# Kernel optimization log

Hardware: AMD Instinct MI355X
Metric: run time of the kernel (lower is better)

Reference implementation:

```python
import jax, jax.numpy as jnp
from jax import lax
import numpy as np

WAY = 100
SHOT = 5
QUERY = 15
D = 4096
LAM = 10.0
ALPHA = 0.2
N_EPOCHS = 20
EPS = 1e-6
MAXITERS = 1000
N_L = WAY * SHOT          # 500 labeled
N_U = WAY * QUERY         # 1500 unlabeled
N_TOT = N_L + N_U         # 2000


def setup_inputs() -> dict:
    key = jax.random.key(0)
    kx, = jax.random.split(key, 1)
    X = jax.random.uniform(kx, (N_TOT, D), dtype=jnp.float32)  # features must be >= 0
    # data is ordered as (shot+query) blocks of `way` samples, one per class
    labels = jnp.tile(jnp.arange(WAY, dtype=jnp.int32), SHOT + QUERY)
    return {"X": X, "labels": labels}


def _normalize(X):
    # F.normalize(p=2, dim=-1) with eps=1e-12
    return X / jnp.maximum(jnp.linalg.norm(X, axis=-1, keepdims=True), 1e-12)


def _cdist(X, Y):
    # Euclidean distances [n, m] via gram trick (avoids [n, m, d] intermediate)
    d2 = (X * X).sum(-1)[:, None] + (Y * Y).sum(-1)[None, :] - 2.0 * (X @ Y.T)
    return jnp.sqrt(jnp.maximum(d2, 1e-12))


def _sinkhorn(M, r, c):
    # Row/col scaling loop of compute_optimal_transport, tracked via scaling
    # vectors (a, b) so P_k = a * K * b exactly matches the in-place updates.
    K = jnp.exp(-LAM * M)
    K = K / K.sum()
    n, m = M.shape

    def step(carry, _):
        a, b, prev, done = carry
        rowsum = a * (K @ b)                       # P.sum(-1)
        err = jnp.max(jnp.abs(prev - rowsum))      # convergence check vs old u
        done = done | (err <= EPS)
        a_new = jnp.where(done, a, a * r / rowsum)
        colsum = b * (K.T @ a_new)                 # P.sum(1) after row scaling
        b_new = jnp.where(done, b, b * c / colsum)
        prev_new = jnp.where(done, prev, rowsum)
        return (a_new, b_new, prev_new, done), None

    init = (jnp.ones(n, M.dtype), jnp.ones(m, M.dtype),
            jnp.zeros(n, M.dtype), jnp.array(False))
    (a, b, _, _), _ = lax.scan(step, init, None, length=MAXITERS)
    return a[:, None] * K * b[None, :]


def _forward(X, labels):
    # power transform
    X = jnp.sqrt(X + 1e-6)
    # scale (mode='val'): normalize -> center labeled/unlabeled separately -> normalize
    X = _normalize(X)
    Xl = X[:N_L] - X[:N_L].mean(0, keepdims=True)
    Xu = X[N_L:] - X[N_L:].mean(0, keepdims=True)
    Z = _normalize(jnp.concatenate([Xl, Xu], axis=0))

    # init class means from labeled shots
    mus0 = Z.reshape(SHOT + QUERY, WAY, -1)[:SHOT].mean(0)  # [way, d]

    r = jnp.ones(N_U, Z.dtype)
    c = jnp.full((WAY,), float(QUERY), Z.dtype)
    onehot = jax.nn.one_hot(labels[:N_L], WAY, dtype=Z.dtype)

    def get_probas(mus):
        dist = _cdist(Z, mus)                      # [n_tot, way]
        Pu = _sinkhorn(dist[N_L:], r, c)           # [n_u, way]
        return jnp.concatenate([onehot, Pu], axis=0)

    def epoch(mus, _):
        p = get_probas(mus)
        emus = (p.T @ Z) / p.sum(0)[:, None]       # estimate_from_mask
        return mus + ALPHA * (emus - mus), None    # update_from_estimate

    mus, _ = lax.scan(epoch, mus0, None, length=N_EPOCHS)

    P = get_probas(mus)
    logP = jnp.log(P[N_L:] + 1e-5)
    acc = (jnp.argmax(P[N_L:], axis=-1) == labels[N_L:]).astype(jnp.float32).mean()
    return logP, acc


def reference(X, labels):
    return _forward(X, labels)
```

## Files before the change

### kernel.cpp

```cpp
#include <hip/hip_runtime.h>

#define WAY   100
#define SHOT  5
#define NQ    15
#define DD    4096
#define N_L   500
#define N_U   1500
#define N_TOT 2000
#define LAMF  10.0f
#define EPSF  1e-6f
#define MAXIT 1000

#define OFF_Z      0u
#define OFF_CPP    3145728u
#define OFF_MEANL  8192000u
#define OFF_MEANU  8196096u
#define OFF_SL     8200192u
#define OFF_MUSA   8609792u
#define OFF_MUSB   9068544u
#define OFF_MUSQP  9527296u
#define OFF_MUSB16 9552896u
#define OFF_PTH    9782272u
#define OFF_PTL    9868288u
#define OFF_KMAT   9954304u
#define OFF_COLS   10104320u
#define OFF_MISC   10113920u
#define OFF_ZUT    10114688u
#define OFF_ZUTL   13260416u
#define OFF_AG     16406144u
#define OFF_PREVG  16407680u
#define OFF_BINIT  16409216u

#define SINK_BLOCKS 16
#define SINK_T 512
#define RPB 94
#define CPR 12
#define PTS 1536
#define CPS 409600u

typedef __attribute__((ext_vector_type(8))) short short8_t;
typedef __attribute__((ext_vector_type(4))) float f32x4;

__device__ __forceinline__ short f2bs(float f) {
  unsigned u = __float_as_uint(f);
  unsigned r = (u + 0x7FFFu + ((u >> 16) & 1u)) >> 16;
  return (short)r;
}
__device__ __forceinline__ float bs2f(short s) {
  return __uint_as_float(((unsigned)(unsigned short)s) << 16);
}

__device__ __forceinline__ float ld_agent(const float* p) {
  return __hip_atomic_load(p, __ATOMIC_RELAXED, __HIP_MEMORY_SCOPE_AGENT);
}
__device__ __forceinline__ void st_agent(float* p, float v) {
  __hip_atomic_store(p, v, __ATOMIC_RELAXED, __HIP_MEMORY_SCOPE_AGENT);
}

__global__ __launch_bounds__(256) void k_pow_norm(const float* __restrict__ X, float* __restrict__ Z,
                                                  float* __restrict__ msums, unsigned* __restrict__ misc_u,
                                                  float* __restrict__ aG) {
  int i = blockIdx.x, tid = threadIdx.x;
  __shared__ float red[256];
  if (i < 32) msums[i * 256 + tid] = 0.f;
  if (i == 32) { misc_u[tid] = 0u; misc_u[tid + 256] = 0u; misc_u[tid + 512] = 0u; }
  if (i == 33) { for (int z = tid; z < 1504; z += 256) aG[z] = -1.f; }
  const float* x = X + (size_t)i * DD;
  float s = 0.f;
  for (int k = tid; k < DD; k += 256) s += x[k] + 1e-6f;
  red[tid] = s; __syncthreads();
  for (int o = 128; o > 0; o >>= 1) { if (tid < o) red[tid] += red[tid + o]; __syncthreads(); }
  float inv = 1.0f / fmaxf(sqrtf(red[0]), 1e-12f);
  float* z = Z + (size_t)i * DD;
  for (int k = tid; k < DD; k += 256) z[k] = sqrtf(x[k] + 1e-6f) * inv;
}

__global__ __launch_bounds__(256) void k_colmeans(const float* __restrict__ Z, float* __restrict__ mLs,
                                                  float* __restrict__ mUs) {
  int k = blockIdx.x * 256 + threadIdx.x;
  int r0 = blockIdx.y * 80;
  float sL = 0.f, sU = 0.f;
  for (int r = r0; r < r0 + 80; ++r) {
    float v = Z[(size_t)r * DD + k];
    if (r < N_L) sL += v; else sU += v;
  }
  if (r0 < N_L) atomicAdd(&mLs[k], sL);
  if (r0 + 80 > N_L) atomicAdd(&mUs[k], sU);
}

__global__ __launch_bounds__(256) void k_center(float* __restrict__ Z, const float* __restrict__ mLs,
                                                const float* __restrict__ mUs) {
  int i = blockIdx.x, tid = threadIdx.x;
  __shared__ float red[256];
  const float* m = (i < N_L) ? mLs : mUs;
  const float scale = (i < N_L) ? (1.0f / 500.0f) : (1.0f / 1500.0f);
  float* z = Z + (size_t)i * DD;
  float s = 0.f;
  for (int k = tid; k < DD; k += 256) { float v = z[k] - m[k] * scale; s += v * v; }
  red[tid] = s; __syncthreads();
  for (int o = 128; o > 0; o >>= 1) { if (tid < o) red[tid] += red[tid + o]; __syncthreads(); }
  float inv = 1.0f / fmaxf(sqrtf(red[0]), 1e-12f);
  for (int k = tid; k < DD; k += 256) z[k] = (z[k] - m[k] * scale) * inv;
}

__global__ __launch_bounds__(256) void k_musinit(const float* __restrict__ Z, float* __restrict__ SL,
                                                 float* __restrict__ mus, short* __restrict__ musb,
                                                 float* __restrict__ musqP, float* __restrict__ binit) {
  int w = blockIdx.x, tid = threadIdx.x;
  __shared__ float red[256];
  if (tid == 0) binit[w] = 1.0f;
  float q = 0.f;
  for (int k = tid; k < DD; k += 256) {
    float s = 0.f;
    for (int sh = 0; sh < SHOT; ++sh) s += Z[(size_t)(sh * WAY + w) * DD + k];
    SL[(size_t)w * DD + k] = s;
    float m = s / 5.0f;
    mus[(size_t)w * DD + k] = m;
    musb[(size_t)w * DD + k] = f2bs(m);
    q += m * m;
  }
  red[tid] = q; __syncthreads();
  for (int o = 128; o > 0; o >>= 1) { if (tid < o) red[tid] += red[tid + o]; __syncthreads(); }
  if (tid == 0) musqP[(size_t)w * 256] = red[0];
  else musqP[(size_t)w * 256 + tid] = 0.f;
}

__global__ __launch_bounds__(256) void k_zb(const float* __restrict__ Z, short* __restrict__ Zb, int ubase) {
  size_t i0 = (size_t)ubase * DD + ((size_t)blockIdx.x * 256 + threadIdx.x) * 8;
  short8_t v;
  if (i0 < (size_t)N_U * DD) {
    const float* src = Z + (size_t)N_L * DD + i0;
    float4 a = *(const float4*)src;
    float4 b = *(const float4*)(src + 4);
    v[0] = f2bs(a.x); v[1] = f2bs(a.y); v[2] = f2bs(a.z); v[3] = f2bs(a.w);
    v[4] = f2bs(b.x); v[5] = f2bs(b.y); v[6] = f2bs(b.z); v[7] = f2bs(b.w);
  } else {
    v = (short8_t){0, 0, 0, 0, 0, 0, 0, 0};
  }
  *(short8_t*)(Zb + i0) = v;
}

__global__ __launch_bounds__(256) void k_zt(const float* __restrict__ Z, short* __restrict__ ZTH,
                                            short* __restrict__ ZTL) {
  __shared__ float tile[32][33];
  int k0 = blockIdx.x * 32, u0 = blockIdx.y * 32;
  int c = threadIdx.x & 31, r0 = threadIdx.x >> 5;
#pragma unroll
  for (int rr = 0; rr < 4; ++rr) {
    int r = r0 + rr * 8;
    int u = u0 + r;
    tile[r][c] = (u < N_U) ? Z[(size_t)(N_L + u) * DD + k0 + c] : 0.f;
  }
  __syncthreads();
#pragma unroll
  for (int rr = 0; rr < 4; ++rr) {
    int r = r0 + rr * 8;
    float v = tile[c][r];
    short hi = f2bs(v);
    ZTH[(size_t)(k0 + r) * PTS + u0 + c] = hi;
    ZTL[(size_t)(k0 + r) * PTS + u0 + c] = f2bs(v - bs2f(hi));
  }
}

__global__ __launch_bounds__(256) void k_gemm1K(const short* __restrict__ Zb, const short* __restrict__ musb,
                                                const float* __restrict__ musqP, float* __restrict__ Kmat,
                                                unsigned* __restrict__ misc_u) {
  int tid = threadIdx.x;
  __shared__ float redA[4 * 7 * 4 * 64];
  __shared__ float musq2[2][128];
  if (blockIdx.x == 0) {
    for (int z = tid; z < 768; z += 256) misc_u[z] = 0u;
  }
  {
    int w = tid >> 1, half = tid & 1;
    if (w < WAY) {
      const float* mp = musqP + (size_t)w * 256 + half * 128;
      float q = 0.f;
#pragma unroll 4
      for (int bb = 0; bb < 128; bb += 4) {
        float4 v4 = *(const float4*)(mp + bb);
        q += (v4.x + v4.y) + (v4.z + v4.w);
      }
      musq2[half][w] = q;
    }
  }
  int wv = tid >> 6, l = tid & 63;
  int l15 = l & 15, quad = (l >> 4) & 3;
  int u0 = blockIdx.x * 16;
  f32x4 acc[7];
#pragma unroll
  for (int c = 0; c < 7; ++c) acc[c] = (f32x4){0.f, 0.f, 0.f, 0.f};

  const short* bp = Zb + (size_t)(u0 + l15) * DD + wv * 1024 + quad * 8;
  const short* ap = musb + (size_t)l15 * DD + wv * 1024 + quad * 8;
#pragma unroll 2
  for (int kc = 0; kc < 1024; kc += 32) {
    short8_t bf = *(const short8_t*)(bp + kc);
#pragma unroll
    for (int c = 0; c < 7; ++c) {
      short8_t af = *(const short8_t*)(ap + (size_t)c * 16 * DD + kc);
      acc[c] = __builtin_amdgcn_mfma_f32_16x16x32_bf16(af, bf, acc[c], 0, 0, 0);
    }
  }
#pragma unroll
  for (int c = 0; c < 7; ++c)
#pragma unroll
    for (int r = 0; r < 4; ++r)
      redA[((wv * 7 + c) * 4 + r) * 64 + l] = acc[c][r];
  __syncthreads();
  if (wv == 0) {
    int u = u0 + l15;
#pragma unroll
    for (int c = 0; c < 7; ++c)
#pragma unroll
      for (int r = 0; r < 4; ++r) {
        int base = (c * 4 + r) * 64 + l;
        float s = redA[base] + redA[base + 1792] + redA[base + 3584] + redA[base + 5376];
        int w = 16 * c + quad * 4 + r;
        if (w < WAY && u < N_U) {
          float d2 = 1.0f + (musq2[0][w] + musq2[1][w]) - 2.0f * s;
          Kmat[(size_t)u * WAY + w] = expf(-LAMF * sqrtf(fmaxf(d2, 1e-12f)));
        }
      }
  }
}

__device__ __forceinline__ void gbar(unsigned* slots, unsigned t) {
  __syncthreads();
  if (threadIdx.x == 0) {
    asm volatile("s_waitcnt vmcnt(0) lgkmcnt(0)" ::: "memory");
    __hip_atomic_store(slots + (unsigned)blockIdx.x * 16, t, __ATOMIC_RELAXED, __HIP_MEMORY_SCOPE_AGENT);
  }
  if (threadIdx.x < SINK_BLOCKS) {
    while (__hip_atomic_load(slots + threadIdx.x * 16, __ATOMIC_ACQUIRE, __HIP_MEMORY_SCOPE_AGENT) < t)
      __builtin_amdgcn_s_sleep(1);
  }
  __syncthreads();
}

__global__ __launch_bounds__(SINK_T) void k_sink(const float* __restrict__ Kg,
                                                 short* __restrict__ PTH, short* __restrict__ PTL,
                                                 float* __restrict__ colsP, float* __restrict__ aG,
                                                 float* __restrict__ prevG, float* __restrict__ binit,
                                                 unsigned* __restrict__ misc_u, float* __restrict__ misc_f,
                                                 const int* __restrict__ labels, float* __restrict__ out,
                                                 int finalmode) {
  __shared__ float Kl[RPB * 100];
  __shared__ float4 bS4[25];
  __shared__ float a[RPB], aold[RPB], prevs[RPB];
  __shared__ float rerr[SINK_T];
  __shared__ float c2[800];
  __shared__ float red[SINK_T];
  __shared__ float eSh;
  float* bS = (float*)bS4;
  unsigned* slots = misc_u + 8;
  float* KsumG = misc_f + 3;
  int tid = threadIdx.x;
  int row0 = (int)blockIdx.x * RPB;
  int nrows = (blockIdx.x == SINK_BLOCKS - 1) ? (N_U - row0) : RPB;

  float ks = 0.f;
  int n4 = nrows * 25;
  const float4* Ksrc = (const float4*)(Kg + (size_t)row0 * 100);
  for (int i = tid; i < n4; i += SINK_T) {
    float4 v = Ksrc[i];
    *(float4*)(&Kl[i * 4]) = v;
    ks += (v.x + v.y) + (v.z + v.w);
  }
  red[tid] = ks; __syncthreads();
  for (int o = SINK_T / 2; o > 0; o >>= 1) { if (tid < o) red[tid] += red[tid + o]; __syncthreads(); }
  if (tid == 0) atomicAdd(KsumG, red[0]);
  if (tid < WAY) bS[tid] = binit[tid];

  bool warm = (aG[row0] >= 0.f);
  unsigned bt = 0;
  if (!warm) { ++bt; gbar(slots, bt); }
  float S = warm ? 1.f : ld_agent(KsumG);
  if (tid < nrows) {
    a[tid] = warm ? aG[row0 + tid] : (1.0f / S);
    prevs[tid] = warm ? prevG[row0 + tid] : 0.f;
  }

  bool conv = false;
  for (int t = 0; t < MAXIT; ++t) {
    float* cp = colsP + (t & 1) * 2048;
    __syncthreads();
    if (tid < nrows) {
      const float* kr = &Kl[tid * 100];
      float4 ac = {0.f, 0.f, 0.f, 0.f};
#pragma unroll
      for (int j4 = 0; j4 < 25; ++j4) {
        float4 bv = bS4[j4];
        float4 kv = *(const float4*)(kr + j4 * 4);
        ac.x = fmaf(kv.x, bv.x, ac.x); ac.y = fmaf(kv.y, bv.y, ac.y);
        ac.z = fmaf(kv.z, bv.z, ac.z); ac.w = fmaf(kv.w, bv.w, ac.w);
      }
      float rs = ((ac.x + ac.y) + (ac.z + ac.w)) * a[tid];
      rerr[tid] = fabsf(prevs[tid] - rs);
      aold[tid] = a[tid];
      a[tid] = a[tid] / rs;
      prevs[tid] = rs;
    } else {
      rerr[tid] = 0.f;
    }
    __syncthreads();
    if (tid < 200) {
      int j4 = tid % 25, ch = tid / 25;
      int rlo = ch * CPR, rhi = rlo + CPR; if (rhi > nrows) rhi = nrows;
      float4 pa = {0.f, 0.f, 0.f, 0.f};
      for (int r = rlo; r < rhi; ++r) {
        float4 kv = *(const float4*)(&Kl[r * 100 + j4 * 4]);
        float av = a[r];
        pa.x = fmaf(kv.x, av, pa.x); pa.y = fmaf(kv.y, av, pa.y);
        pa.z = fmaf(kv.z, av, pa.z); pa.w = fmaf(kv.w, av, pa.w);
      }
      *(float4*)(&c2[ch * 100 + j4 * 4]) = pa;
    }
    if (tid >= 448) {
      int t6 = tid & 63;
      float m = rerr[t6];
#pragma unroll
      for (int k = 1; k < 8; ++k) m = fmaxf(m, rerr[t6 + 64 * k]);
#pragma unroll
      for (int o = 32; o > 0; o >>= 1) m = fmaxf(m, __shfl_down(m, o));
      if (t6 == 0) st_agent(cp + (unsigned)blockIdx.x * 128 + 100, m);
    }
    __syncthreads();
    if (tid < WAY) {
      float s = ((c2[tid] + c2[100 + tid]) + (c2[200 + tid] + c2[300 + tid])) +
                ((c2[400 + tid] + c2[500 + tid]) + (c2[600 + tid] + c2[700 + tid]));
      st_agent(cp + (unsigned)blockIdx.x * 128 + tid, s);
    }
    ++bt;
    gbar(slots, bt);
    float bnew = 0.f;
    if (tid >= 256 && tid < 256 + WAY) {
      int j = tid - 256;
      float s = 0.f;
#pragma unroll
      for (int sb = 0; sb < SINK_BLOCKS; ++sb) s += ld_agent(cp + sb * 128 + j);
      bnew = (float)NQ / s;
    }
    if (tid < 64) {
      float e = (tid < SINK_BLOCKS) ? ld_agent(cp + tid * 128 + 100) : 0.f;
#pragma unroll
      for (int o = 8; o > 0; o >>= 1) e = fmaxf(e, __shfl_down(e, o));
      if (tid == 0) eSh = e;
    }
    __syncthreads();
    if (eSh <= EPSF) { conv = true; break; }
    if (tid >= 256 && tid < 256 + WAY) bS[tid - 256] = bnew;
  }
  __syncthreads();

  if (finalmode) {
    for (int idx = tid; idx < nrows * WAY; idx += SINK_T) {
      int r = idx / WAY, j = idx - r * WAY;
      float av = conv ? aold[r] : a[r];
      float p = av * Kl[r * 100 + j] * bS[j];
      out[(size_t)(row0 + r) * WAY + j] = logf(p + 1e-5f);
    }
    if (tid < nrows) {
      const float* kr = &Kl[tid * 100];
      int am = 0; float bv = kr[0] * bS[0];
      for (int j = 1; j < WAY; ++j) { float p = kr[j] * bS[j]; if (p > bv) { bv = p; am = j; } }
      if (am == labels[N_L + row0 + tid]) atomicAdd(misc_u + 5, 1u);
    }
    return;
  }

  if (tid < nrows) {
    float af = conv ? aold[tid] : a[tid];
    aG[row0 + tid] = af;
    prevG[row0 + tid] = prevs[tid];
  }
  if (blockIdx.x == 0 && tid < WAY) binit[tid] = bS[tid];
  for (int idx = tid; idx < WAY * nrows; idx += SINK_T) {
    int j = idx / nrows; int r = idx - j * nrows;
    float av = conv ? aold[r] : a[r];
    float p = av * Kl[r * 100 + j] * bS[j];
    short hi = f2bs(p);
    PTH[(size_t)j * PTS + row0 + r] = hi;
    PTL[(size_t)j * PTS + row0 + r] = f2bs(p - bs2f(hi));
  }
  if (blockIdx.x == SINK_BLOCKS - 1) {
    for (int idx = tid; idx < WAY * 4; idx += SINK_T) {
      int j = idx >> 2;
      PTH[(size_t)j * PTS + 1500 + (idx & 3)] = 0;
      PTL[(size_t)j * PTS + 1500 + (idx & 3)] = 0;
    }
  }
}

__global__ __launch_bounds__(64) void k_gemm2(const short* __restrict__ PTH, const short* __restrict__ PTL,
                                              const short* __restrict__ ZTH, const short* __restrict__ ZTL,
                                              float* __restrict__ CPp) {
  int l = threadIdx.x, l15 = l & 15, quad = l >> 4;
  int k0 = blockIdx.x * 16;
  int us = blockIdx.y;
  int kcb = us * 192;
  int kce = (us == 7) ? 1504 : kcb + 192;
  f32x4 acc[7];
#pragma unroll
  for (int c = 0; c < 7; ++c) acc[c] = (f32x4){0.f, 0.f, 0.f, 0.f};
  size_t aoff = (size_t)l15 * PTS + quad * 8;
  const short* bph = ZTH + (size_t)(k0 + l15) * PTS + quad * 8;
  const short* bpl = ZTL + (size_t)(k0 + l15) * PTS + quad * 8;
  for (int kc = kcb; kc < kce; kc += 32) {
    short8_t bh = *(const short8_t*)(bph + kc);
    short8_t bl = *(const short8_t*)(bpl + kc);
#pragma unroll
    for (int c = 0; c < 7; ++c) {
      short8_t ah = *(const short8_t*)(PTH + aoff + (size_t)c * 16 * PTS + kc);
      short8_t al = *(const short8_t*)(PTL + aoff + (size_t)c * 16 * PTS + kc);
      acc[c] = __builtin_amdgcn_mfma_f32_16x16x32_bf16(ah, bh, acc[c], 0, 0, 0);
      acc[c] = __builtin_amdgcn_mfma_f32_16x16x32_bf16(al, bh, acc[c], 0, 0, 0);
      acc[c] = __builtin_amdgcn_mfma_f32_16x16x32_bf16(ah, bl, acc[c], 0, 0, 0);
    }
  }
  float* dst = CPp + (size_t)us * CPS;
#pragma unroll
  for (int c = 0; c < 7; ++c)
#pragma unroll
    for (int r = 0; r < 4; ++r) {
      int w = 16 * c + quad * 4 + r;
      if (w < WAY) dst[(size_t)w * DD + k0 + l15] = acc[c][r];
    }
}

__global__ __launch_bounds__(256) void k_musup(const float* __restrict__ musR, const float* __restrict__ SL,
                                               const float* __restrict__ CPp, float* __restrict__ musW,
                                               short* __restrict__ musb, float* __restrict__ musqP) {
  int w = blockIdx.x, tid = threadIdx.x;
  int kb = blockIdx.y * 1024;
  __shared__ float red[256];
  float q = 0.f;
  for (int k = kb + tid; k < kb + 1024; k += 256) {
    size_t o = (size_t)w * DD + k;
    float c = 0.f;
#pragma unroll
    for (int s = 0; s < 8; ++s) c += CPp[(size_t)s * CPS + o];
    float emus = (SL[o] + c) / 20.0f;
    float m = musR[o];
    float v = m + 0.2f * (emus - m);
    musW[o] = v;
    musb[o] = f2bs(v);
    q += v * v;
  }
  red[tid] = q; __syncthreads();
  for (int o = 128; o > 0; o >>= 1) { if (tid < o) red[tid] += red[tid + o]; __syncthreads(); }
  if (tid == 0) musqP[(size_t)w * 256 + blockIdx.y] = red[0];
}

__global__ void k_acc(const unsigned* __restrict__ ctr, float* __restrict__ out) {
  if (threadIdx.x == 0) out[N_U * WAY] = (float)(*ctr) / 1500.0f;
}

extern "C" void kernel_launch(void* const* d_in, const int* in_sizes, int n_in,
                              void* d_out, int out_size, void* d_ws, size_t ws_size,
                              hipStream_t stream) {
  const float* X = (const float*)d_in[0];
  const int* labels = (const int*)d_in[1];
  float* out = (float*)d_out;
  float* ws = (float*)d_ws;

  float* Z     = ws + OFF_Z;
  short* Zb    = (short*)(ws + OFF_Z);
  float* CPp   = ws + OFF_CPP;
  float* meanL = ws + OFF_MEANL;
  float* meanU = ws + OFF_MEANU;
  float* SL    = ws + OFF_SL;
  float* musA  = ws + OFF_MUSA;
  float* musB  = ws + OFF_MUSB;
  float* musqP = ws + OFF_MUSQP;
  short* musb16 = (short*)(ws + OFF_MUSB16);
  short* PTH   = (short*)(ws + OFF_PTH);
  short* PTL   = (short*)(ws + OFF_PTL);
  float* Kmat  = ws + OFF_KMAT;
  float* colsP = ws + OFF_COLS;
  float* misc_f = ws + OFF_MISC;
  unsigned* misc_u = (unsigned*)(ws + OFF_MISC);
  short* ZTH   = (short*)(ws + OFF_ZUT);
  short* ZTL   = (short*)(ws + OFF_ZUTL);
  float* aG    = ws + OFF_AG;
  float* prevG = ws + OFF_PREVG;
  float* binit = ws + OFF_BINIT;

  k_pow_norm<<<N_TOT, 256, 0, stream>>>(X, Z, meanL, misc_u, aG);
  k_colmeans<<<dim3(16, 25), 256, 0, stream>>>(Z, meanL, meanU);
  k_center<<<N_TOT, 256, 0, stream>>>(Z, meanL, meanU);
  k_musinit<<<WAY, 256, 0, stream>>>(Z, SL, musA, musb16, musqP, binit);
  k_zt<<<dim3(128, 48), 256, 0, stream>>>(Z, ZTH, ZTL);
  k_zb<<<1536, 256, 0, stream>>>(Z, Zb, 0);
  k_zb<<<1536, 256, 0, stream>>>(Z, Zb, 768);

  float* musR = musA;
  float* musW = musB;
  for (int e = 0; e < 20; ++e) {
    k_gemm1K<<<96, 256, 0, stream>>>(Zb, musb16, musqP, Kmat, misc_u);
    k_sink<<<SINK_BLOCKS, SINK_T, 0, stream>>>(Kmat, PTH, PTL, colsP, aG, prevG, binit, misc_u, misc_f,
                                               labels, out, 0);
    k_gemm2<<<dim3(256, 8), 64, 0, stream>>>(PTH, PTL, ZTH, ZTL, CPp);
    k_musup<<<dim3(WAY, 4), 256, 0, stream>>>(musR, SL, CPp, musW, musb16, musqP);
    float* tmp = musR; musR = musW; musW = tmp;
  }
  k_gemm1K<<<96, 256, 0, stream>>>(Zb, musb16, musqP, Kmat, misc_u);
  k_sink<<<SINK_BLOCKS, SINK_T, 0, stream>>>(Kmat, PTH, PTL, colsP, aG, prevG, binit, misc_u, misc_f,
                                             labels, out, 1);
  k_acc<<<1, 64, 0, stream>>>(misc_u + 5, out);
}
```

Baseline: 1.966 ms.

## Fuse mean update into gemm2 via last-tile counter and halve Sinkhorn blocks

The separate k_musup launch is removed. Each k_gemm2 tile writes its partial with agent-scope stores and bumps a per-column-tile atomic counter, and the last of the 8 split-K blocks reduces the partials, updates the class means and writes the per-tile squared-norm partials. Separately, the Sinkhorn kernel now runs on 8 blocks of 188 rows each instead of 16 blocks of 94, so each of its up to 1000 grid-wide barriers synchronises fewer blocks. The costs are serialized tail work in one block per tile, less parallelism in the Sinkhorn row pass, and reliance on the counters being reset and on musqP now holding 256 partials per class instead of 4.

```diff
diff --git a/kernel.cpp b/kernel.cpp
--- a/kernel.cpp
+++ b/kernel.cpp
@@ -31,10 +31,10 @@
 #define OFF_PREVG  16407680u
 #define OFF_BINIT  16409216u
 
-#define SINK_BLOCKS 16
+#define SINK_BLOCKS 8
 #define SINK_T 512
-#define RPB 94
-#define CPR 12
+#define RPB 188
+#define CPR 24
 #define PTS 1536
 #define CPS 409600u
 
@@ -283,7 +283,7 @@
 
   bool conv = false;
   for (int t = 0; t < MAXIT; ++t) {
-    float* cp = colsP + (t & 1) * 2048;
+    float* cp = colsP + (t & 1) * 1024;
     __syncthreads();
     if (tid < nrows) {
       const float* kr = &Kl[tid * 100];
@@ -344,7 +344,7 @@
     if (tid < 64) {
       float e = (tid < SINK_BLOCKS) ? ld_agent(cp + tid * 128 + 100) : 0.f;
 #pragma unroll
-      for (int o = 8; o > 0; o >>= 1) e = fmaxf(e, __shfl_down(e, o));
+      for (int o = 4; o > 0; o >>= 1) e = fmaxf(e, __shfl_down(e, o));
       if (tid == 0) eSh = e;
     }
     __syncthreads();
@@ -394,7 +394,10 @@
 
 __global__ __launch_bounds__(64) void k_gemm2(const short* __restrict__ PTH, const short* __restrict__ PTL,
                                               const short* __restrict__ ZTH, const short* __restrict__ ZTL,
-                                              float* __restrict__ CPp) {
+                                              float* __restrict__ CPp,
+                                              const float* __restrict__ musR, const float* __restrict__ SL,
+                                              float* __restrict__ musW, short* __restrict__ musb,
+                                              float* __restrict__ musqP, unsigned* __restrict__ tilec) {
   int l = threadIdx.x, l15 = l & 15, quad = l >> 4;
   int k0 = blockIdx.x * 16;
   int us = blockIdx.y;
@@ -424,32 +427,30 @@
 #pragma unroll
     for (int r = 0; r < 4; ++r) {
       int w = 16 * c + quad * 4 + r;
-      if (w < WAY) dst[(size_t)w * DD + k0 + l15] = acc[c][r];
-    }
-}
-
-__global__ __launch_bounds__(256) void k_musup(const float* __restrict__ musR, const float* __restrict__ SL,
-                                               const float* __restrict__ CPp, float* __restrict__ musW,
-                                               short* __restrict__ musb, float* __restrict__ musqP) {
-  int w = blockIdx.x, tid = threadIdx.x;
-  int kb = blockIdx.y * 1024;
-  __shared__ float red[256];
-  float q = 0.f;
-  for (int k = kb + tid; k < kb + 1024; k += 256) {
-    size_t o = (size_t)w * DD + k;
-    float c = 0.f;
-#pragma unroll
-    for (int s = 0; s < 8; ++s) c += CPp[(size_t)s * CPS + o];
-    float emus = (SL[o] + c) / 20.0f;
+      if (w < WAY) st_agent(&dst[(size_t)w * DD + k0 + l15], acc[c][r]);
+    }
+  asm volatile("s_waitcnt vmcnt(0)" ::: "memory");
+  unsigned old = 0u;
+  if (l == 0) old = atomicAdd(&tilec[blockIdx.x], 1u);
+  old = __shfl(old, 0);
+  if (old != 7u) return;
+  int kk = k0 + l15;
+  int g = l >> 4;
+  for (int w = g; w < WAY; w += 4) {
+    size_t o = (size_t)w * DD + kk;
+    float cacc = 0.f;
+#pragma unroll
+    for (int s = 0; s < 8; ++s) cacc += ld_agent(&CPp[(size_t)s * CPS + o]);
+    float emus = (SL[o] + cacc) / 20.0f;
     float m = musR[o];
     float v = m + 0.2f * (emus - m);
     musW[o] = v;
     musb[o] = f2bs(v);
-    q += v * v;
-  }
-  red[tid] = q; __syncthreads();
-  for (int o = 128; o > 0; o >>= 1) { if (tid < o) red[tid] += red[tid + o]; __syncthreads(); }
-  if (tid == 0) musqP[(size_t)w * 256 + blockIdx.y] = red[0];
+    float vsq = v * v;
+#pragma unroll
+    for (int o2 = 8; o2 > 0; o2 >>= 1) vsq += __shfl_xor(vsq, o2);
+    if (l15 == 0) musqP[(size_t)w * 256 + blockIdx.x] = vsq;
+  }
 }
 
 __global__ void k_acc(const unsigned* __restrict__ ctr, float* __restrict__ out) {
@@ -500,8 +501,8 @@
     k_gemm1K<<<96, 256, 0, stream>>>(Zb, musb16, musqP, Kmat, misc_u);
     k_sink<<<SINK_BLOCKS, SINK_T, 0, stream>>>(Kmat, PTH, PTL, colsP, aG, prevG, binit, misc_u, misc_f,
                                                labels, out, 0);
-    k_gemm2<<<dim3(256, 8), 64, 0, stream>>>(PTH, PTL, ZTH, ZTL, CPp);
-    k_musup<<<dim3(WAY, 4), 256, 0, stream>>>(musR, SL, CPp, musW, musb16, musqP);
+    k_gemm2<<<dim3(256, 8), 64, 0, stream>>>(PTH, PTL, ZTH, ZTL, CPp, musR, SL, musW, musb16, musqP,
+                                             misc_u + 512);
     float* tmp = musR; musR = musW; musW = tmp;
   }
   k_gemm1K<<<96, 256, 0, stream>>>(Zb, musb16, musqP, Kmat, misc_u);
```

Measured after the change: 2.635 ms. 1.34x slower.
